# Kernel tuning notes

Measured on AMD Instinct MI355X. Metric: run time of the kernel, lower is better.

The kernel has to match this reference:

```python
import jax, jax.numpy as jnp
import numpy as np

B, S, L, D = 32, 8, 128, 768
A, T = 10, 8
VOCAB = 1000


def setup_inputs() -> dict:
    key = jax.random.key(0)
    k1, k2, k3, k4, k5 = jax.random.split(key, 5)
    sentence_ids = jax.random.randint(k1, (B, S, L), 0, VOCAB)
    sentence_attention_masks = jnp.ones((B, S, L), dtype=jnp.float32)
    # precomputed sum of last 4 BERT hidden layers (backbone excluded)
    sentence_embeddings = jax.random.normal(k2, (B, S, L, D), dtype=jnp.float32)
    predicate_ids = jax.random.randint(k3, (B, S, A, T), 0, VOCAB)
    arg0_ids = jax.random.randint(k4, (B, S, A, T), 0, VOCAB)
    arg1_ids = jax.random.randint(k5, (B, S, A, T), 0, VOCAB)
    return {
        "sentence_ids": sentence_ids,
        "sentence_attention_masks": sentence_attention_masks,
        "sentence_embeddings": sentence_embeddings,
        "predicate_ids": predicate_ids,
        "arg0_ids": arg0_ids,
        "arg1_ids": arg1_ids,
    }


def _mean_pool(emb, mask):
    # emb: [b,s,l,d], mask: [b,s,l] -> [b,s,d]
    masked_sum = jnp.einsum('bsld,bsl->bsd', emb, mask)
    counts = jnp.clip(mask.sum(-1, keepdims=True), 1, None)
    return masked_sum / counts


def _arg_embedding(arg_ids, sentence_ids, emb):
    # arg_ids: [b,s,a,t] int, sentence_ids: [b,s,l] int, emb: [b,s,l,d]
    # match[b,s,a,t,l] = sentence token l equals arg token t (and arg token != 0)
    match = (sentence_ids[:, :, None, None, :] == arg_ids[..., None]) & (arg_ids[..., None] != 0)
    mf = match.astype(emb.dtype)
    counts = mf.sum(-1)                                   # [b,s,a,t]
    summed = jnp.einsum('bsatl,bsld->bsatd', mf, emb)      # [b,s,a,t,d]
    avg = summed / jnp.maximum(counts, 1.0)[..., None]
    has = counts > 0                                       # [b,s,a,t]
    t_dim = arg_ids.shape[-1]
    # original loop overwrites per token -> keep the LAST token with a match
    last = (t_dim - 1) - jnp.argmax(has[..., ::-1], axis=-1)  # [b,s,a]
    sel = jnp.take_along_axis(avg, last[..., None, None], axis=3)[:, :, :, 0, :]
    valid = has.any(-1)                                    # [b,s,a]
    return jnp.where(valid[..., None], sel, jnp.zeros((), emb.dtype))


def reference(sentence_ids, sentence_attention_masks, sentence_embeddings,
              predicate_ids, arg0_ids, arg1_ids):
    sentence_embeddings_avg = _mean_pool(sentence_embeddings, sentence_attention_masks)
    predicate_embeddings = _arg_embedding(predicate_ids, sentence_ids, sentence_embeddings)
    arg0_embeddings = _arg_embedding(arg0_ids, sentence_ids, sentence_embeddings)
    arg1_embeddings = _arg_embedding(arg1_ids, sentence_ids, sentence_embeddings)
    return (sentence_embeddings_avg, predicate_embeddings, arg0_embeddings, arg1_embeddings)
```

## Files before the change

### kernel.cpp

```cpp
#include <hip/hip_runtime.h>

#define Bq 32
#define Sq 8
#define Lq 128
#define Dq 768
#define Aq 10
#define Tq 8

constexpr int D4   = Dq / 4;
constexpr int NBS  = Bq * Sq;
constexpr int NBSA = NBS * Aq;

__global__ __launch_bounds__(384) void srl_fused_k(
    const int* __restrict__ sids, const float* __restrict__ mask,
    const float* __restrict__ emb, const int* __restrict__ pred,
    const int* __restrict__ a0, const int* __restrict__ a1,
    float* __restrict__ out)
{
    int bs   = blockIdx.x;
    int tid  = threadIdx.x;
    int wv   = tid >> 6;
    int lane = tid & 63;

    if (wv < 3) {
        float mv = mask[(size_t)bs * Lq + lane] +
                   mask[(size_t)bs * Lq + 64 + lane];
        for (int off = 32; off > 0; off >>= 1)
            mv += __shfl_xor(mv, off);
        float inv = 1.0f / fmaxf(mv, 1.0f);

        const float*  mrow = mask + (size_t)bs * Lq;
        const float4* eb   = (const float4*)emb +
                             (size_t)bs * Lq * D4 + wv * 64 + lane;

        float4 acc = make_float4(0.f, 0.f, 0.f, 0.f);
#pragma unroll 16
        for (int l = 0; l < Lq; ++l) {
            float  m = mrow[l];
            float4 v = eb[(size_t)l * D4];
            acc.x += v.x * m; acc.y += v.y * m;
            acc.z += v.z * m; acc.w += v.w * m;
        }
        float4 r = make_float4(acc.x * inv, acc.y * inv,
                               acc.z * inv, acc.w * inv);
        ((float4*)out)[(size_t)bs * D4 + wv * 64 + lane] = r;
        return;
    }

    int set = wv - 3;
    const int* ids = (set == 0) ? pred : ((set == 1) ? a0 : a1);

    int s0 = sids[(size_t)bs * Lq + lane];
    int s1 = sids[(size_t)bs * Lq + 64 + lane];

    const float4* eb = (const float4*)emb + (size_t)bs * Lq * D4;

    for (int a = 0; a < Aq; ++a) {
        int bsa = bs * Aq + a;
        int idv = (lane < Tq) ? ids[(size_t)bsa * Tq + lane] : 0;

        unsigned long long B0 = 0, B1 = 0;
        int ccount = 0;
#pragma unroll
        for (int t = Tq - 1; t >= 0; --t) {
            if (ccount == 0) {
                int idt = __shfl(idv, t);
                if (idt != 0) {
                    unsigned long long b0 = __ballot(s0 == idt);
                    unsigned long long b1 = __ballot(s1 == idt);
                    int c = (int)(__popcll(b0) + __popcll(b1));
                    if (c > 0) { B0 = b0; B1 = b1; ccount = c; }
                }
            }
        }

        float4 acc0 = make_float4(0.f, 0.f, 0.f, 0.f);
        float4 acc1 = acc0, acc2 = acc0;
        unsigned long long b = B0;
        while (b) {
            int l = (int)__builtin_ctzll(b); b &= b - 1;
            float4 v0 = eb[(size_t)l * D4 + lane];
            float4 v1 = eb[(size_t)l * D4 + 64 + lane];
            float4 v2 = eb[(size_t)l * D4 + 128 + lane];
            acc0.x += v0.x; acc0.y += v0.y; acc0.z += v0.z; acc0.w += v0.w;
            acc1.x += v1.x; acc1.y += v1.y; acc1.z += v1.z; acc1.w += v1.w;
            acc2.x += v2.x; acc2.y += v2.y; acc2.z += v2.z; acc2.w += v2.w;
        }
        b = B1;
        while (b) {
            int l = (int)__builtin_ctzll(b) + 64; b &= b - 1;
            float4 v0 = eb[(size_t)l * D4 + lane];
            float4 v1 = eb[(size_t)l * D4 + 64 + lane];
            float4 v2 = eb[(size_t)l * D4 + 128 + lane];
            acc0.x += v0.x; acc0.y += v0.y; acc0.z += v0.z; acc0.w += v0.w;
            acc1.x += v1.x; acc1.y += v1.y; acc1.z += v1.z; acc1.w += v1.w;
            acc2.x += v2.x; acc2.y += v2.y; acc2.z += v2.z; acc2.w += v2.w;
        }

        float inv = (ccount > 0) ? 1.0f / (float)ccount : 0.0f;
        float4* o4 = (float4*)out +
                     ((size_t)NBS + (size_t)set * NBSA + bsa) * D4;
        o4[lane]       = make_float4(acc0.x*inv, acc0.y*inv, acc0.z*inv, acc0.w*inv);
        o4[64 + lane]  = make_float4(acc1.x*inv, acc1.y*inv, acc1.z*inv, acc1.w*inv);
        o4[128 + lane] = make_float4(acc2.x*inv, acc2.y*inv, acc2.z*inv, acc2.w*inv);
    }
}

extern "C" void kernel_launch(void* const* d_in, const int* in_sizes, int n_in,
                              void* d_out, int out_size, void* d_ws, size_t ws_size,
                              hipStream_t stream) {
    const int*   sids = (const int*)d_in[0];
    const float* mask = (const float*)d_in[1];
    const float* emb  = (const float*)d_in[2];
    const int*   pred = (const int*)d_in[3];
    const int*   a0   = (const int*)d_in[4];
    const int*   a1   = (const int*)d_in[5];
    float* out = (float*)d_out;

    srl_fused_k<<<NBS, 384, 0, stream>>>(sids, mask, emb, pred, a0, a1, out);
}
```

Measured before the change: 27.23 us.

## Split mean-pool over four sequence chunks with shared-memory reduction

Raises the block size from 384 to 960 threads. The mean-pool part now uses 12 waves instead of 3: each group of 192 threads sums a 32-row slice of the sequence, using a mask cached in shared memory. The four partial sums are then reduced through shared memory. The goal is more memory loads in flight per CU for the bandwidth-heavy pooling, since there is only one block per (b,s). In exchange it adds barriers that the argument waves must also reach, more shared memory per block, and a register budget tied to the larger block.

```diff
diff --git a/kernel.cpp b/kernel.cpp
--- a/kernel.cpp
+++ b/kernel.cpp
@@ -11,7 +11,7 @@
 constexpr int NBS  = Bq * Sq;
 constexpr int NBSA = NBS * Aq;
 
-__global__ __launch_bounds__(384) void srl_fused_k(
+__global__ __launch_bounds__(960) void srl_fused_k(
     const int* __restrict__ sids, const float* __restrict__ mask,
     const float* __restrict__ emb, const int* __restrict__ pred,
     const int* __restrict__ a0, const int* __restrict__ a1,
@@ -22,32 +22,53 @@
     int wv   = tid >> 6;
     int lane = tid & 63;
 
-    if (wv < 3) {
+    __shared__ float  marr[Lq];
+    __shared__ float4 red[4][D4];
+
+    if (wv < 12) {
+        if (tid < Lq) marr[tid] = mask[(size_t)bs * Lq + tid];
+
         float mv = mask[(size_t)bs * Lq + lane] +
                    mask[(size_t)bs * Lq + 64 + lane];
         for (int off = 32; off > 0; off >>= 1)
             mv += __shfl_xor(mv, off);
         float inv = 1.0f / fmaxf(mv, 1.0f);
 
-        const float*  mrow = mask + (size_t)bs * Lq;
-        const float4* eb   = (const float4*)emb +
-                             (size_t)bs * Lq * D4 + wv * 64 + lane;
+        __syncthreads();
 
+        int g = tid / 192;
+        int c = tid - g * 192;
+
+        const float4* eb = (const float4*)emb +
+                           (size_t)bs * Lq * D4 + (size_t)(g * 32) * D4 + c;
         float4 acc = make_float4(0.f, 0.f, 0.f, 0.f);
 #pragma unroll 16
-        for (int l = 0; l < Lq; ++l) {
-            float  m = mrow[l];
+        for (int l = 0; l < 32; ++l) {
+            float  m = marr[g * 32 + l];
             float4 v = eb[(size_t)l * D4];
             acc.x += v.x * m; acc.y += v.y * m;
             acc.z += v.z * m; acc.w += v.w * m;
         }
-        float4 r = make_float4(acc.x * inv, acc.y * inv,
-                               acc.z * inv, acc.w * inv);
-        ((float4*)out)[(size_t)bs * D4 + wv * 64 + lane] = r;
+        red[g][c] = acc;
+
+        __syncthreads();
+
+        if (tid < D4) {
+            float4 a = red[0][tid], b = red[1][tid];
+            float4 cc = red[2][tid], d = red[3][tid];
+            float4 r;
+            r.x = (a.x + b.x + cc.x + d.x) * inv;
+            r.y = (a.y + b.y + cc.y + d.y) * inv;
+            r.z = (a.z + b.z + cc.z + d.z) * inv;
+            r.w = (a.w + b.w + cc.w + d.w) * inv;
+            ((float4*)out)[(size_t)bs * D4 + tid] = r;
+        }
         return;
     }
 
-    int set = wv - 3;
+    __syncthreads();
+
+    int set = wv - 12;
     const int* ids = (set == 0) ? pred : ((set == 1) ? a0 : a1);
 
     int s0 = sids[(size_t)bs * Lq + lane];
@@ -104,6 +125,8 @@
         o4[64 + lane]  = make_float4(acc1.x*inv, acc1.y*inv, acc1.z*inv, acc1.w*inv);
         o4[128 + lane] = make_float4(acc2.x*inv, acc2.y*inv, acc2.z*inv, acc2.w*inv);
     }
+
+    __syncthreads();
 }
 
 extern "C" void kernel_launch(void* const* d_in, const int* in_sizes, int n_in,
@@ -117,5 +140,5 @@
     const int*   a1   = (const int*)d_in[5];
     float* out = (float*)d_out;
 
-    srl_fused_k<<<NBS, 384, 0, stream>>>(sids, mask, emb, pred, a0, a1, out);
+    srl_fused_k<<<NBS, 960, 0, stream>>>(sids, mask, emb, pred, a0, a1, out);
 }
```

After: 31.52 us. 1.16x slower.
